# Performance work log

Measured on AMD Instinct MI355X. Metric: run time of the kernel, lower is better.

The kernel has to match this reference:

```python
import jax, jax.numpy as jnp
import numpy as np

B, LQ, D = 4, 10000, 256
HEADS, LVLS, PTS = 8, 1, 4
HW = 100
LIN = HW * HW


def setup_inputs() -> dict:
    key = jax.random.key(0)
    ks = jax.random.split(key, 14)
    s = 0.02
    ctr = jax.random.uniform(ks[2], (B, LQ, LVLS, 2), jnp.float32)
    wh = 0.05 + 0.2 * jax.random.uniform(ks[3], (B, LQ, LVLS, 2), jnp.float32)
    return {
        "query": jax.random.normal(ks[0], (B, LQ, D), jnp.float32),
        "reference_points": jnp.concatenate([ctr, wh], axis=-1),
        "input_flatten": jax.random.normal(ks[1], (B, LIN, D), jnp.float32),
        "input_spatial_shapes": jnp.array([[HW, HW]], jnp.int32),
        "input_level_start_index": jnp.zeros((LVLS,), jnp.int32),
        "input_padding_mask": jnp.zeros((B, LIN), jnp.bool_),
        "Wv": s * jax.random.normal(ks[4], (D, D), jnp.float32),
        "bv": jnp.zeros((D,), jnp.float32),
        "Woff": s * jax.random.normal(ks[5], (D, HEADS * LVLS * PTS * 2), jnp.float32),
        "boff": s * jax.random.normal(ks[6], (HEADS * LVLS * PTS * 2,), jnp.float32),
        "Wa": s * jax.random.normal(ks[7], (D, HEADS * LVLS * PTS), jnp.float32),
        "ba": jnp.zeros((HEADS * LVLS * PTS,), jnp.float32),
        "Wout": s * jax.random.normal(ks[8], (D, D), jnp.float32),
        "bout": jnp.zeros((D,), jnp.float32),
    }


def _ms_deform_attn(query, reference_points, input_flatten, input_padding_mask,
                    Wv, bv, Woff, boff, Wa, ba, Wout, bout):
    Bn, Lq, Dm = query.shape
    Lin = input_flatten.shape[1]
    Hh, L, P = HEADS, LVLS, PTS
    Cd = Dm // Hh
    # value projection + padding mask
    value = input_flatten @ Wv + bv
    value = jnp.where(input_padding_mask[..., None], 0.0, value)
    # sampling offsets & attention weights
    off = (query @ Woff + boff).reshape(Bn, Lq, Hh, L, P, 2)
    attn = jax.nn.softmax((query @ Wa + ba).reshape(Bn, Lq, Hh, L * P), axis=-1)
    loc = (reference_points[:, :, None, :, None, :2]
           + off / P * reference_points[:, :, None, :, None, 2:] * 0.5)
    # value -> (B*Hh, Cd, Lin); square single-level map H=W=sqrt(Lin)
    v = value.reshape(Bn, Lin, Hh, Cd).transpose(0, 2, 3, 1).reshape(Bn * Hh, Cd, Lin)
    Hs = int(round(Lin ** 0.5)); Ws = Hs
    # level 0 grid: (B*Hh, Lq, P, 2), normalized to [-1, 1]
    g = (2.0 * loc - 1.0)[:, :, :, 0].transpose(0, 2, 1, 3, 4).reshape(Bn * Hh, Lq, P, 2)
    x = (g[..., 0] + 1.0) * Ws / 2.0 - 0.5
    y = (g[..., 1] + 1.0) * Hs / 2.0 - 0.5
    x0 = jnp.floor(x).astype(jnp.int32); y0 = jnp.floor(y).astype(jnp.int32)
    x1 = x0 + 1; y1 = y0 + 1
    wx = x - x0.astype(x.dtype); wy = y - y0.astype(y.dtype)

    def valid(xi, yi):
        return ((xi >= 0) & (xi < Ws) & (yi >= 0) & (yi < Hs)).astype(value.dtype)

    def gather(xi, yi):
        idx = (jnp.clip(yi, 0, Hs - 1) * Ws + jnp.clip(xi, 0, Ws - 1)).reshape(Bn * Hh, 1, Lq * P)
        out = jnp.take_along_axis(v, jnp.broadcast_to(idx, (Bn * Hh, Cd, Lq * P)), axis=2)
        return out.reshape(Bn * Hh, Cd, Lq, P)

    sv = (gather(x0, y0) * ((1 - wx) * (1 - wy) * valid(x0, y0))[:, None]
          + gather(x0, y1) * ((1 - wx) * wy * valid(x0, y1))[:, None]
          + gather(x1, y0) * (wx * (1 - wy) * valid(x1, y0))[:, None]
          + gather(x1, y1) * (wx * wy * valid(x1, y1))[:, None])  # (B*Hh, Cd, Lq, P)
    aw = attn.transpose(0, 2, 1, 3).reshape(Bn * Hh, 1, Lq, L * P)
    out = (sv * aw).sum(-1).reshape(Bn, Hh * Cd, Lq).transpose(0, 2, 1)  # (B, Lq, D)
    return out @ Wout + bout


def reference(query, reference_points, input_flatten, input_spatial_shapes,
              input_level_start_index, input_padding_mask,
              Wv, bv, Woff, boff, Wa, ba, Wout, bout):
    # input_spatial_shapes / level_start_index are redundant here: the core is
    # single-level with H=W=sqrt(Len_in) (faithful to the source code).
    return _ms_deform_attn(query, reference_points, input_flatten, input_padding_mask,
                           Wv, bv, Woff, boff, Wa, ba, Wout, bout)
```

## Files before the change

kernel.cpp:

```cpp
#include <hip/hip_runtime.h>

#define BATCH 4
#define LQ    10000
#define DM    256
#define NH    8
#define NP    4
#define HWD   100
#define LIN   10000

typedef unsigned short ushort_t;
typedef __attribute__((ext_vector_type(8))) short bf16x8;
typedef __attribute__((ext_vector_type(8))) unsigned short u16x8;
typedef __attribute__((ext_vector_type(4))) float f32x4;

__device__ __forceinline__ unsigned short f2bf(float f) {
    unsigned int u = __float_as_uint(f);
    u += 0x7FFFu + ((u >> 16) & 1u);
    return (unsigned short)(u >> 16);
}

__device__ __forceinline__ void gload16(const ushort_t* g, ushort_t* l) {
    __builtin_amdgcn_global_load_lds(
        (const __attribute__((address_space(1))) void*)g,
        (__attribute__((address_space(3))) void*)l, 16, 0, 0);
}

__global__ __launch_bounds__(256) void prep_kernel(
    const float* __restrict__ Wv, const float* __restrict__ Wout,
    const float* __restrict__ Woff, const float* __restrict__ Wa,
    const float* __restrict__ boff, const float* __restrict__ ba,
    ushort_t* __restrict__ WtV, ushort_t* __restrict__ WtO,
    ushort_t* __restrict__ Wcomb, float* __restrict__ bcomb)
{
    const int n = blockIdx.x, k = threadIdx.x;
    const int t = k >> 6, lc = (k >> 3) & 7, j = k & 7;
    const int ct = lc ^ ((n >> 1) & 7);
    const size_t addr = (size_t)n * 256 + t * 64 + ct * 8 + j;
    if (blockIdx.y == 0) {
        WtV[addr] = f2bf(Wv[(size_t)k * 256 + n]);
    } else if (blockIdx.y == 1) {
        WtO[addr] = f2bf(Wout[(size_t)k * 256 + n]);
    } else if (n < 96) {
        float w = (n < 64) ? Woff[(size_t)k * 64 + n] : Wa[(size_t)k * 32 + (n - 64)];
        Wcomb[addr] = f2bf(w);
        if (k == 0) bcomb[n] = (n < 64) ? boff[n] : ba[n - 64];
    }
}

__global__ __launch_bounds__(256) void gemm_in_kernel(
    const float* __restrict__ flat, const float* __restrict__ query,
    const ushort_t* __restrict__ WtV, const ushort_t* __restrict__ Wcomb,
    const float* __restrict__ bv, const float* __restrict__ bcomb,
    ushort_t* __restrict__ value, float* __restrict__ oaproj)
{
    __shared__ ushort_t As[64 * 64];
    __shared__ ushort_t Bs[256 * 64];

    const int tid  = threadIdx.x;
    const int lane = tid & 63;
    const int wv   = tid >> 6;

    const int ar  = tid >> 2;
    const int akb = tid & 3;
    const int as_ = (ar >> 1) & 7;
    const int fr = lane & 15, kb = lane >> 4;
    const int ln8 = lane >> 3, lc8 = lane & 7;

    if (blockIdx.x < 625) {
        const int row0 = blockIdx.x * 64;
        const f32x4 zero = {0.f, 0.f, 0.f, 0.f};
        f32x4 acc[4][4];
        #pragma unroll
        for (int m = 0; m < 4; ++m)
            #pragma unroll
            for (int n = 0; n < 4; ++n) acc[m][n] = zero;

        for (int k0 = 0; k0 < 256; k0 += 64) {
            const int t = k0 >> 6;
            #pragma unroll
            for (int it = 0; it < 8; ++it) {
                int r0 = (it * 4 + wv) * 8;
                gload16(&WtV[(size_t)(r0 + ln8) * 256 + t * 64 + lc8 * 8],
                        &Bs[r0 * 64]);
            }
            {
                const float* p = &flat[(size_t)(row0 + ar) * 256 + k0 + akb * 8];
                float4 f0 = *reinterpret_cast<const float4*>(p);
                float4 f1 = *reinterpret_cast<const float4*>(p + 4);
                u16x8 pk;
                pk[0] = f2bf(f0.x); pk[1] = f2bf(f0.y);
                pk[2] = f2bf(f0.z); pk[3] = f2bf(f0.w);
                pk[4] = f2bf(f1.x); pk[5] = f2bf(f1.y);
                pk[6] = f2bf(f1.z); pk[7] = f2bf(f1.w);
                *reinterpret_cast<u16x8*>(&As[ar * 64 + ((akb ^ as_) * 8)]) = pk;
                f0 = *reinterpret_cast<const float4*>(p + 32);
                f1 = *reinterpret_cast<const float4*>(p + 36);
                pk[0] = f2bf(f0.x); pk[1] = f2bf(f0.y);
                pk[2] = f2bf(f0.z); pk[3] = f2bf(f0.w);
                pk[4] = f2bf(f1.x); pk[5] = f2bf(f1.y);
                pk[6] = f2bf(f1.z); pk[7] = f2bf(f1.w);
                *reinterpret_cast<u16x8*>(&As[ar * 64 + (((akb + 4) ^ as_) * 8)]) = pk;
            }
            __syncthreads();

            #pragma unroll
            for (int ks = 0; ks < 2; ++ks) {
                const int lc = ks * 4 + kb;
                bf16x8 af[4], bf[4];
                #pragma unroll
                for (int m = 0; m < 4; ++m) {
                    int r = m * 16 + fr;
                    af[m] = *reinterpret_cast<const bf16x8*>(
                        &As[r * 64 + ((lc ^ ((r >> 1) & 7)) * 8)]);
                }
                #pragma unroll
                for (int n = 0; n < 4; ++n) {
                    int c = wv * 64 + n * 16 + fr;
                    bf[n] = *reinterpret_cast<const bf16x8*>(
                        &Bs[c * 64 + ((lc ^ ((c >> 1) & 7)) * 8)]);
                }
                #pragma unroll
                for (int m = 0; m < 4; ++m)
                    #pragma unroll
                    for (int n = 0; n < 4; ++n)
                        acc[m][n] = __builtin_amdgcn_mfma_f32_16x16x32_bf16(
                            af[m], bf[n], acc[m][n], 0, 0, 0);
            }
            __syncthreads();
        }

        #pragma unroll
        for (int n = 0; n < 4; ++n) {
            int c = wv * 64 + n * 16 + fr;
            float bb = bv[c];
            int hh = c >> 5, ch = c & 31;
            #pragma unroll
            for (int m = 0; m < 4; ++m) {
                #pragma unroll
                for (int j = 0; j < 4; ++j) {
                    int r = row0 + m * 16 + kb * 4 + j;
                    int rb = (int)((unsigned)r / 10000u);
                    int pix = r - rb * 10000;
                    size_t addr = (((size_t)(rb * 8 + hh)) * LIN + pix) * 32 + ch;
                    value[addr] = f2bf(acc[m][n][j] + bb);
                }
            }
        }
    } else {
        const int row0 = (blockIdx.x - 625) * 64;
        const f32x4 zero = {0.f, 0.f, 0.f, 0.f};
        f32x4 acc[6];
        #pragma unroll
        for (int n = 0; n < 6; ++n) acc[n] = zero;

        for (int k0 = 0; k0 < 256; k0 += 64) {
            const int t = k0 >> 6;
            #pragma unroll
            for (int it = 0; it < 3; ++it) {
                int r0 = (it * 4 + wv) * 8;
                gload16(&Wcomb[(size_t)(r0 + ln8) * 256 + t * 64 + lc8 * 8],
                        &Bs[r0 * 64]);
            }
            {
                const float* p = &query[(size_t)(row0 + ar) * 256 + k0 + akb * 8];
                float4 f0 = *reinterpret_cast<const float4*>(p);
                float4 f1 = *reinterpret_cast<const float4*>(p + 4);
                u16x8 pk;
                pk[0] = f2bf(f0.x); pk[1] = f2bf(f0.y);
                pk[2] = f2bf(f0.z); pk[3] = f2bf(f0.w);
                pk[4] = f2bf(f1.x); pk[5] = f2bf(f1.y);
                pk[6] = f2bf(f1.z); pk[7] = f2bf(f1.w);
                *reinterpret_cast<u16x8*>(&As[ar * 64 + ((akb ^ as_) * 8)]) = pk;
                f0 = *reinterpret_cast<const float4*>(p + 32);
                f1 = *reinterpret_cast<const float4*>(p + 36);
                pk[0] = f2bf(f0.x); pk[1] = f2bf(f0.y);
                pk[2] = f2bf(f0.z); pk[3] = f2bf(f0.w);
                pk[4] = f2bf(f1.x); pk[5] = f2bf(f1.y);
                pk[6] = f2bf(f1.z); pk[7] = f2bf(f1.w);
                *reinterpret_cast<u16x8*>(&As[ar * 64 + (((akb + 4) ^ as_) * 8)]) = pk;
            }
            __syncthreads();

            #pragma unroll
            for (int ks = 0; ks < 2; ++ks) {
                const int lc = ks * 4 + kb;
                bf16x8 af;
                {
                    int r = wv * 16 + fr;
                    af = *reinterpret_cast<const bf16x8*>(
                        &As[r * 64 + ((lc ^ ((r >> 1) & 7)) * 8)]);
                }
                #pragma unroll
                for (int n = 0; n < 6; ++n) {
                    int c = n * 16 + fr;
                    bf16x8 bf = *reinterpret_cast<const bf16x8*>(
                        &Bs[c * 64 + ((lc ^ ((c >> 1) & 7)) * 8)]);
                    acc[n] = __builtin_amdgcn_mfma_f32_16x16x32_bf16(
                        af, bf, acc[n], 0, 0, 0);
                }
            }
            __syncthreads();
        }

        #pragma unroll
        for (int n = 0; n < 6; ++n) {
            int c = n * 16 + fr;
            float bb = bcomb[c];
            #pragma unroll
            for (int j = 0; j < 4; ++j) {
                int r = row0 + wv * 16 + kb * 4 + j;
                oaproj[(size_t)r * 96 + c] = acc[n][j] + bb;
            }
        }
    }
}

__global__ __launch_bounds__(256, 4) void deform_kernel(
    const float* __restrict__ oaproj, const float* __restrict__ refpts,
    const ushort_t* __restrict__ value, ushort_t* __restrict__ out)
{
    __shared__ int4   soff[NP * 64];
    __shared__ float4 swt [NP * 64];

    const int blk = blockIdx.x;
    const int xcd = blk & 7;
    const int sub = (blk >> 3) & 3;
    const int chunk = blk >> 5;
    const int map = xcd * 4 + sub;
    const int b = map >> 3, h = map & 7;
    const int q0 = chunk * 64;

    const int tid = threadIdx.x;

    if (tid < 64) {
        const int qg = q0 + tid;
        if (qg >= LQ) {
            int4 zi = {0, 0, 0, 0};
            float4 zf = {0.f, 0.f, 0.f, 0.f};
            #pragma unroll
            for (int p = 0; p < NP; ++p) { soff[p * 64 + tid] = zi; swt[p * 64 + tid] = zf; }
        } else {
            const size_t row = (size_t)b * LQ + qg;
            const float* oa = oaproj + row * 96;
            float4 l4 = *reinterpret_cast<const float4*>(oa + 64 + h * 4);
            float mx = fmaxf(fmaxf(l4.x, l4.y), fmaxf(l4.z, l4.w));
            float e0 = __expf(l4.x - mx), e1 = __expf(l4.y - mx);
            float e2 = __expf(l4.z - mx), e3 = __expf(l4.w - mx);
            float inv = 1.f / (e0 + e1 + e2 + e3);
            float ew[4] = {e0 * inv, e1 * inv, e2 * inv, e3 * inv};
            float4 o0 = *reinterpret_cast<const float4*>(oa + h * 8);
            float4 o1 = *reinterpret_cast<const float4*>(oa + h * 8 + 4);
            float oxv[4] = {o0.x, o0.z, o1.x, o1.z};
            float oyv[4] = {o0.y, o0.w, o1.y, o1.w};
            const float* rp = refpts + row * 4;
            float cx = rp[0], cy = rp[1], rw = rp[2], rh = rp[3];
            #pragma unroll
            for (int p = 0; p < NP; ++p) {
                float x = (cx + oxv[p] * rw * 0.125f) * (float)HWD - 0.5f;
                float y = (cy + oyv[p] * rh * 0.125f) * (float)HWD - 0.5f;
                float x0f = floorf(x), y0f = floorf(y);
                float wx = x - x0f, wy = y - y0f;
                int x0 = (int)x0f, y0 = (int)y0f;
                int x1 = x0 + 1, y1 = y0 + 1;
                float vx0 = (x0 >= 0 && x0 < HWD) ? 1.f : 0.f;
                float vx1 = (x1 >= 0 && x1 < HWD) ? 1.f : 0.f;
                float vy0 = (y0 >= 0 && y0 < HWD) ? 1.f : 0.f;
                float vy1 = (y1 >= 0 && y1 < HWD) ? 1.f : 0.f;
                int cx0 = min(max(x0, 0), HWD - 1), cx1 = min(max(x1, 0), HWD - 1);
                int cy0 = min(max(y0, 0), HWD - 1), cy1 = min(max(y1, 0), HWD - 1);
                float aw = ew[p];
                int4 of = {cy0 * HWD + cx0, cy0 * HWD + cx1,
                           cy1 * HWD + cx0, cy1 * HWD + cx1};
                float4 wt = {aw * (1.f - wx) * (1.f - wy) * vx0 * vy0,
                             aw * wx * (1.f - wy) * vx1 * vy0,
                             aw * (1.f - wx) * wy * vx0 * vy1,
                             aw * wx * wy * vx1 * vy1};
                soff[p * 64 + tid] = of;
                swt [p * 64 + tid] = wt;
            }
        }
    }
    __syncthreads();

    const int q = tid >> 2, c8 = tid & 3;
    const int qg = q0 + q;
    const ushort_t* vb = value + (size_t)map * (LIN * 32) + c8 * 8;

    int4 of[4]; float4 w4[4];
    #pragma unroll
    for (int p = 0; p < NP; ++p) {
        of[p] = soff[p * 64 + q];
        w4[p] = swt [p * 64 + q];
    }
    uint4 vv[4][4];
    #pragma unroll
    for (int p = 0; p < NP; ++p) {
        vv[p][0] = *reinterpret_cast<const uint4*>(vb + ((size_t)of[p].x << 5));
        vv[p][1] = *reinterpret_cast<const uint4*>(vb + ((size_t)of[p].y << 5));
        vv[p][2] = *reinterpret_cast<const uint4*>(vb + ((size_t)of[p].z << 5));
        vv[p][3] = *reinterpret_cast<const uint4*>(vb + ((size_t)of[p].w << 5));
    }
    float a0 = 0.f, a1 = 0.f, a2 = 0.f, a3 = 0.f;
    float a4 = 0.f, a5 = 0.f, a6 = 0.f, a7 = 0.f;
    #define ACC(V, W) { const float w_ = (W); const uint4 v_ = (V); \
        a0 += w_ * __uint_as_float(v_.x << 16); \
        a1 += w_ * __uint_as_float(v_.x & 0xffff0000u); \
        a2 += w_ * __uint_as_float(v_.y << 16); \
        a3 += w_ * __uint_as_float(v_.y & 0xffff0000u); \
        a4 += w_ * __uint_as_float(v_.z << 16); \
        a5 += w_ * __uint_as_float(v_.z & 0xffff0000u); \
        a6 += w_ * __uint_as_float(v_.w << 16); \
        a7 += w_ * __uint_as_float(v_.w & 0xffff0000u); }
    #pragma unroll
    for (int p = 0; p < NP; ++p) {
        ACC(vv[p][0], w4[p].x);
        ACC(vv[p][1], w4[p].y);
        ACC(vv[p][2], w4[p].z);
        ACC(vv[p][3], w4[p].w);
    }
    #undef ACC

    if (qg < LQ) {
        const size_t orow = (size_t)b * LQ + qg;
        u16x8 pk;
        pk[0] = f2bf(a0); pk[1] = f2bf(a1);
        pk[2] = f2bf(a2); pk[3] = f2bf(a3);
        pk[4] = f2bf(a4); pk[5] = f2bf(a5);
        pk[6] = f2bf(a6); pk[7] = f2bf(a7);
        const int cc = h * 4 + c8;
        const int t = cc >> 3;
        const int ct = (cc & 7) ^ ((int)(orow >> 1) & 7);
        *reinterpret_cast<u16x8*>(&out[orow * 256 + t * 64 + ct * 8]) = pk;
    }
}

__global__ __launch_bounds__(256) void gemm_out_kernel(
    const ushort_t* __restrict__ A, const ushort_t* __restrict__ Wt,
    const float* __restrict__ bias, float* __restrict__ Cout)
{
    __shared__ ushort_t As[64 * 64];
    __shared__ ushort_t Bs[256 * 64];

    const int tid  = threadIdx.x;
    const int lane = tid & 63;
    const int wv   = tid >> 6;
    const int row0 = blockIdx.x * 64;

    const f32x4 zero = {0.f, 0.f, 0.f, 0.f};
    f32x4 acc[4][4];
    #pragma unroll
    for (int m = 0; m < 4; ++m)
        #pragma unroll
        for (int n = 0; n < 4; ++n) acc[m][n] = zero;

    const int fr = lane & 15, kb = lane >> 4;
    const int ln8 = lane >> 3, lc8 = lane & 7;

    for (int k0 = 0; k0 < 256; k0 += 64) {
        const int t = k0 >> 6;
        #pragma unroll
        for (int it = 0; it < 2; ++it) {
            int r0 = (it * 4 + wv) * 8;
            gload16(&A[(size_t)(row0 + r0 + ln8) * 256 + t * 64 + lc8 * 8],
                    &As[r0 * 64]);
        }
        #pragma unroll
        for (int it = 0; it < 8; ++it) {
            int r0 = (it * 4 + wv) * 8;
            gload16(&Wt[(size_t)(r0 + ln8) * 256 + t * 64 + lc8 * 8],
                    &Bs[r0 * 64]);
        }
        __syncthreads();

        #pragma unroll
        for (int ks = 0; ks < 2; ++ks) {
            const int lc = ks * 4 + kb;
            bf16x8 af[4], bf[4];
            #pragma unroll
            for (int m = 0; m < 4; ++m) {
                int r = m * 16 + fr;
                af[m] = *reinterpret_cast<const bf16x8*>(
                    &As[r * 64 + ((lc ^ ((r >> 1) & 7)) * 8)]);
            }
            #pragma unroll
            for (int n = 0; n < 4; ++n) {
                int c = wv * 64 + n * 16 + fr;
                bf[n] = *reinterpret_cast<const bf16x8*>(
                    &Bs[c * 64 + ((lc ^ ((c >> 1) & 7)) * 8)]);
            }
            #pragma unroll
            for (int m = 0; m < 4; ++m)
                #pragma unroll
                for (int n = 0; n < 4; ++n)
                    acc[m][n] = __builtin_amdgcn_mfma_f32_16x16x32_bf16(
                        af[m], bf[n], acc[m][n], 0, 0, 0);
        }
        __syncthreads();
    }

    #pragma unroll
    for (int m = 0; m < 4; ++m) {
        #pragma unroll
        for (int n = 0; n < 4; ++n) {
            int c = wv * 64 + n * 16 + fr;
            float bb = bias[c];
            #pragma unroll
            for (int j = 0; j < 4; ++j) {
                int r = row0 + m * 16 + kb * 4 + j;
                Cout[(size_t)r * 256 + c] = acc[m][n][j] + bb;
            }
        }
    }
}

extern "C" void kernel_launch(void* const* d_in, const int* in_sizes, int n_in,
                              void* d_out, int out_size, void* d_ws, size_t ws_size,
                              hipStream_t stream)
{
    const float* query  = (const float*)d_in[0];
    const float* refpts = (const float*)d_in[1];
    const float* flat   = (const float*)d_in[2];
    const float* Wv   = (const float*)d_in[6];
    const float* bv   = (const float*)d_in[7];
    const float* Woff = (const float*)d_in[8];
    const float* boff = (const float*)d_in[9];
    const float* Wa   = (const float*)d_in[10];
    const float* ba   = (const float*)d_in[11];
    const float* Wout = (const float*)d_in[12];
    const float* bout = (const float*)d_in[13];
    float* out = (float*)d_out;

    const size_t MROWS = (size_t)BATCH * LIN;
    ushort_t* value  = (ushort_t*)d_ws;
    ushort_t* ws2    = value + MROWS * DM;
    ushort_t* WtV    = ws2 + MROWS * DM;
    ushort_t* WtO    = WtV + 256 * 256;
    ushort_t* Wcomb  = WtO + 256 * 256;
    float*    bcomb  = (float*)(Wcomb + 96 * 256);
    float*    oaproj = bcomb + 128;

    dim3 blk(256);

    prep_kernel<<<dim3(256, 3), blk, 0, stream>>>(
        Wv, Wout, Woff, Wa, boff, ba, WtV, WtO, Wcomb, bcomb);

    gemm_in_kernel<<<dim3(1250), blk, 0, stream>>>(
        flat, query, WtV, Wcomb, bv, bcomb, value, oaproj);

    deform_kernel<<<dim3(157 * 32), blk, 0, stream>>>(
        oaproj, refpts, value, ws2);

    gemm_out_kernel<<<dim3(MROWS / 64), blk, 0, stream>>>(
        ws2, WtO, bout, out);
}
```

Baseline: 72.71 us.

## Double-buffer GEMM K-tiles with 32-wide LDS stages and prefetch

Converts the input-projection and output-projection GEMMs from single-buffered 64-wide K tiles with two barriers per step to double-buffered 32-wide K tiles. The next tile's global loads are issued before the MFMAs on the current one, so memory latency overlaps compute and one barrier per step is dropped. The weight pre-swizzle and the sampler's output layout change to the 32-wide swizzle to match. This adds more loop iterations and barriers in total, and keeps LDS usage the same.

```diff
diff --git a/kernel.cpp b/kernel.cpp
--- a/kernel.cpp
+++ b/kernel.cpp
@@ -33,9 +33,9 @@
     ushort_t* __restrict__ Wcomb, float* __restrict__ bcomb)
 {
     const int n = blockIdx.x, k = threadIdx.x;
-    const int t = k >> 6, lc = (k >> 3) & 7, j = k & 7;
-    const int ct = lc ^ ((n >> 1) & 7);
-    const size_t addr = (size_t)n * 256 + t * 64 + ct * 8 + j;
+    const int t32 = k >> 5, lc = (k >> 3) & 3, j = k & 7;
+    const int ct = lc ^ ((n >> 1) & 3);
+    const size_t addr = (size_t)n * 256 + t32 * 32 + ct * 8 + j;
     if (blockIdx.y == 0) {
         WtV[addr] = f2bf(Wv[(size_t)k * 256 + n]);
     } else if (blockIdx.y == 1) {
@@ -53,8 +53,8 @@
     const float* __restrict__ bv, const float* __restrict__ bcomb,
     ushort_t* __restrict__ value, float* __restrict__ oaproj)
 {
-    __shared__ ushort_t As[64 * 64];
-    __shared__ ushort_t Bs[256 * 64];
+    __shared__ ushort_t As[2][64 * 32];
+    __shared__ ushort_t Bs[2][256 * 32];
 
     const int tid  = threadIdx.x;
     const int lane = tid & 63;
@@ -62,12 +62,13 @@
 
     const int ar  = tid >> 2;
     const int akb = tid & 3;
-    const int as_ = (ar >> 1) & 7;
+    const int asw = (akb ^ ((ar >> 1) & 3)) * 8;
     const int fr = lane & 15, kb = lane >> 4;
-    const int ln8 = lane >> 3, lc8 = lane & 7;
+    const int ln4 = lane >> 2, lc4 = lane & 3;
 
     if (blockIdx.x < 625) {
         const int row0 = blockIdx.x * 64;
+        const float* ap = &flat[(size_t)(row0 + ar) * 256 + akb * 8];
         const f32x4 zero = {0.f, 0.f, 0.f, 0.f};
         f32x4 acc[4][4];
         #pragma unroll
@@ -75,65 +76,74 @@
             #pragma unroll
             for (int n = 0; n < 4; ++n) acc[m][n] = zero;
 
-        for (int k0 = 0; k0 < 256; k0 += 64) {
-            const int t = k0 >> 6;
-            #pragma unroll
-            for (int it = 0; it < 8; ++it) {
-                int r0 = (it * 4 + wv) * 8;
-                gload16(&WtV[(size_t)(r0 + ln8) * 256 + t * 64 + lc8 * 8],
-                        &Bs[r0 * 64]);
-            }
-            {
-                const float* p = &flat[(size_t)(row0 + ar) * 256 + k0 + akb * 8];
-                float4 f0 = *reinterpret_cast<const float4*>(p);
-                float4 f1 = *reinterpret_cast<const float4*>(p + 4);
+        {
+            float4 f0 = *reinterpret_cast<const float4*>(ap);
+            float4 f1 = *reinterpret_cast<const float4*>(ap + 4);
+            u16x8 pk;
+            pk[0] = f2bf(f0.x); pk[1] = f2bf(f0.y);
+            pk[2] = f2bf(f0.z); pk[3] = f2bf(f0.w);
+            pk[4] = f2bf(f1.x); pk[5] = f2bf(f1.y);
+            pk[6] = f2bf(f1.z); pk[7] = f2bf(f1.w);
+            *reinterpret_cast<u16x8*>(&As[0][ar * 32 + asw]) = pk;
+            #pragma unroll
+            for (int it = 0; it < 4; ++it) {
+                int r0 = (it * 4 + wv) * 16;
+                gload16(&WtV[(size_t)(r0 + ln4) * 256 + lc4 * 8], &Bs[0][r0 * 32]);
+            }
+        }
+        __syncthreads();
+
+        int c = 0;
+        for (int t = 0; t < 8; ++t) {
+            const int kn = (t + 1) * 32;
+            const bool pf = (t < 7);
+            float4 f0, f1;
+            if (pf) {
+                f0 = *reinterpret_cast<const float4*>(ap + kn);
+                f1 = *reinterpret_cast<const float4*>(ap + kn + 4);
+                #pragma unroll
+                for (int it = 0; it < 4; ++it) {
+                    int r0 = (it * 4 + wv) * 16;
+                    gload16(&WtV[(size_t)(r0 + ln4) * 256 + kn + lc4 * 8],
+                            &Bs[c ^ 1][r0 * 32]);
+                }
+            }
+            bf16x8 af[4], bf[4];
+            #pragma unroll
+            for (int m = 0; m < 4; ++m) {
+                int r = m * 16 + fr;
+                af[m] = *reinterpret_cast<const bf16x8*>(
+                    &As[c][r * 32 + ((kb ^ ((r >> 1) & 3)) * 8)]);
+            }
+            #pragma unroll
+            for (int n = 0; n < 4; ++n) {
+                int cc = wv * 64 + n * 16 + fr;
+                bf[n] = *reinterpret_cast<const bf16x8*>(
+                    &Bs[c][cc * 32 + ((kb ^ ((cc >> 1) & 3)) * 8)]);
+            }
+            #pragma unroll
+            for (int m = 0; m < 4; ++m)
+                #pragma unroll
+                for (int n = 0; n < 4; ++n)
+                    acc[m][n] = __builtin_amdgcn_mfma_f32_16x16x32_bf16(
+                        af[m], bf[n], acc[m][n], 0, 0, 0);
+            if (pf) {
                 u16x8 pk;
                 pk[0] = f2bf(f0.x); pk[1] = f2bf(f0.y);
                 pk[2] = f2bf(f0.z); pk[3] = f2bf(f0.w);
                 pk[4] = f2bf(f1.x); pk[5] = f2bf(f1.y);
                 pk[6] = f2bf(f1.z); pk[7] = f2bf(f1.w);
-                *reinterpret_cast<u16x8*>(&As[ar * 64 + ((akb ^ as_) * 8)]) = pk;
-                f0 = *reinterpret_cast<const float4*>(p + 32);
-                f1 = *reinterpret_cast<const float4*>(p + 36);
-                pk[0] = f2bf(f0.x); pk[1] = f2bf(f0.y);
-                pk[2] = f2bf(f0.z); pk[3] = f2bf(f0.w);
-                pk[4] = f2bf(f1.x); pk[5] = f2bf(f1.y);
-                pk[6] = f2bf(f1.z); pk[7] = f2bf(f1.w);
-                *reinterpret_cast<u16x8*>(&As[ar * 64 + (((akb + 4) ^ as_) * 8)]) = pk;
+                *reinterpret_cast<u16x8*>(&As[c ^ 1][ar * 32 + asw]) = pk;
             }
             __syncthreads();
-
-            #pragma unroll
-            for (int ks = 0; ks < 2; ++ks) {
-                const int lc = ks * 4 + kb;
-                bf16x8 af[4], bf[4];
-                #pragma unroll
-                for (int m = 0; m < 4; ++m) {
-                    int r = m * 16 + fr;
-                    af[m] = *reinterpret_cast<const bf16x8*>(
-                        &As[r * 64 + ((lc ^ ((r >> 1) & 7)) * 8)]);
-                }
-                #pragma unroll
-                for (int n = 0; n < 4; ++n) {
-                    int c = wv * 64 + n * 16 + fr;
-                    bf[n] = *reinterpret_cast<const bf16x8*>(
-                        &Bs[c * 64 + ((lc ^ ((c >> 1) & 7)) * 8)]);
-                }
-                #pragma unroll
-                for (int m = 0; m < 4; ++m)
-                    #pragma unroll
-                    for (int n = 0; n < 4; ++n)
-                        acc[m][n] = __builtin_amdgcn_mfma_f32_16x16x32_bf16(
-                            af[m], bf[n], acc[m][n], 0, 0, 0);
-            }
-            __syncthreads();
+            c ^= 1;
         }
 
         #pragma unroll
         for (int n = 0; n < 4; ++n) {
-            int c = wv * 64 + n * 16 + fr;
-            float bb = bv[c];
-            int hh = c >> 5, ch = c & 31;
+            int cc = wv * 64 + n * 16 + fr;
+            float bb = bv[cc];
+            int hh = cc >> 5, ch = cc & 31;
             #pragma unroll
             for (int m = 0; m < 4; ++m) {
                 #pragma unroll
@@ -148,68 +158,80 @@
         }
     } else {
         const int row0 = (blockIdx.x - 625) * 64;
+        const float* ap = &query[(size_t)(row0 + ar) * 256 + akb * 8];
         const f32x4 zero = {0.f, 0.f, 0.f, 0.f};
         f32x4 acc[6];
         #pragma unroll
         for (int n = 0; n < 6; ++n) acc[n] = zero;
 
-        for (int k0 = 0; k0 < 256; k0 += 64) {
-            const int t = k0 >> 6;
-            #pragma unroll
-            for (int it = 0; it < 3; ++it) {
-                int r0 = (it * 4 + wv) * 8;
-                gload16(&Wcomb[(size_t)(r0 + ln8) * 256 + t * 64 + lc8 * 8],
-                        &Bs[r0 * 64]);
-            }
+        {
+            float4 f0 = *reinterpret_cast<const float4*>(ap);
+            float4 f1 = *reinterpret_cast<const float4*>(ap + 4);
+            u16x8 pk;
+            pk[0] = f2bf(f0.x); pk[1] = f2bf(f0.y);
+            pk[2] = f2bf(f0.z); pk[3] = f2bf(f0.w);
+            pk[4] = f2bf(f1.x); pk[5] = f2bf(f1.y);
+            pk[6] = f2bf(f1.z); pk[7] = f2bf(f1.w);
+            *reinterpret_cast<u16x8*>(&As[0][ar * 32 + asw]) = pk;
+            #pragma unroll
+            for (int it = 0; it < 2; ++it) {
+                int r0 = (it * 4 + wv) * 16;
+                if (r0 < 96)
+                    gload16(&Wcomb[(size_t)(r0 + ln4) * 256 + lc4 * 8], &Bs[0][r0 * 32]);
+            }
+        }
+        __syncthreads();
+
+        int c = 0;
+        for (int t = 0; t < 8; ++t) {
+            const int kn = (t + 1) * 32;
+            const bool pf = (t < 7);
+            float4 f0, f1;
+            if (pf) {
+                f0 = *reinterpret_cast<const float4*>(ap + kn);
+                f1 = *reinterpret_cast<const float4*>(ap + kn + 4);
+                #pragma unroll
+                for (int it = 0; it < 2; ++it) {
+                    int r0 = (it * 4 + wv) * 16;
+                    if (r0 < 96)
+                        gload16(&Wcomb[(size_t)(r0 + ln4) * 256 + kn + lc4 * 8],
+                                &Bs[c ^ 1][r0 * 32]);
+                }
+            }
+            bf16x8 af;
             {
-                const float* p = &query[(size_t)(row0 + ar) * 256 + k0 + akb * 8];
-                float4 f0 = *reinterpret_cast<const float4*>(p);
-                float4 f1 = *reinterpret_cast<const float4*>(p + 4);
+                int r = wv * 16 + fr;
+                af = *reinterpret_cast<const bf16x8*>(
+                    &As[c][r * 32 + ((kb ^ ((r >> 1) & 3)) * 8)]);
+            }
+            #pragma unroll
+            for (int n = 0; n < 6; ++n) {
+                int cc = n * 16 + fr;
+                bf16x8 bf = *reinterpret_cast<const bf16x8*>(
+                    &Bs[c][cc * 32 + ((kb ^ ((cc >> 1) & 3)) * 8)]);
+                acc[n] = __builtin_amdgcn_mfma_f32_16x16x32_bf16(
+                    af, bf, acc[n], 0, 0, 0);
+            }
+            if (pf) {
                 u16x8 pk;
                 pk[0] = f2bf(f0.x); pk[1] = f2bf(f0.y);
                 pk[2] = f2bf(f0.z); pk[3] = f2bf(f0.w);
                 pk[4] = f2bf(f1.x); pk[5] = f2bf(f1.y);
                 pk[6] = f2bf(f1.z); pk[7] = f2bf(f1.w);
-                *reinterpret_cast<u16x8*>(&As[ar * 64 + ((akb ^ as_) * 8)]) = pk;
-                f0 = *reinterpret_cast<const float4*>(p + 32);
-                f1 = *reinterpret_cast<const float4*>(p + 36);
-                pk[0] = f2bf(f0.x); pk[1] = f2bf(f0.y);
-                pk[2] = f2bf(f0.z); pk[3] = f2bf(f0.w);
-                pk[4] = f2bf(f1.x); pk[5] = f2bf(f1.y);
-                pk[6] = f2bf(f1.z); pk[7] = f2bf(f1.w);
-                *reinterpret_cast<u16x8*>(&As[ar * 64 + (((akb + 4) ^ as_) * 8)]) = pk;
+                *reinterpret_cast<u16x8*>(&As[c ^ 1][ar * 32 + asw]) = pk;
             }
             __syncthreads();
-
-            #pragma unroll
-            for (int ks = 0; ks < 2; ++ks) {
-                const int lc = ks * 4 + kb;
-                bf16x8 af;
-                {
-                    int r = wv * 16 + fr;
-                    af = *reinterpret_cast<const bf16x8*>(
-                        &As[r * 64 + ((lc ^ ((r >> 1) & 7)) * 8)]);
-                }
-                #pragma unroll
-                for (int n = 0; n < 6; ++n) {
-                    int c = n * 16 + fr;
-                    bf16x8 bf = *reinterpret_cast<const bf16x8*>(
-                        &Bs[c * 64 + ((lc ^ ((c >> 1) & 7)) * 8)]);
-                    acc[n] = __builtin_amdgcn_mfma_f32_16x16x32_bf16(
-                        af, bf, acc[n], 0, 0, 0);
-                }
-            }
-            __syncthreads();
+            c ^= 1;
         }
 
         #pragma unroll
         for (int n = 0; n < 6; ++n) {
-            int c = n * 16 + fr;
-            float bb = bcomb[c];
+            int cc = n * 16 + fr;
+            float bb = bcomb[cc];
             #pragma unroll
             for (int j = 0; j < 4; ++j) {
                 int r = row0 + wv * 16 + kb * 4 + j;
-                oaproj[(size_t)r * 96 + c] = acc[n][j] + bb;
+                oaproj[(size_t)r * 96 + cc] = acc[n][j] + bb;
             }
         }
     }
@@ -328,9 +350,9 @@
         pk[4] = f2bf(a4); pk[5] = f2bf(a5);
         pk[6] = f2bf(a6); pk[7] = f2bf(a7);
         const int cc = h * 4 + c8;
-        const int t = cc >> 3;
-        const int ct = (cc & 7) ^ ((int)(orow >> 1) & 7);
-        *reinterpret_cast<u16x8*>(&out[orow * 256 + t * 64 + ct * 8]) = pk;
+        const int t32 = cc >> 2;
+        const int ct = (cc & 3) ^ ((int)(orow >> 1) & 3);
+        *reinterpret_cast<u16x8*>(&out[orow * 256 + t32 * 32 + ct * 8]) = pk;
     }
 }
 
@@ -338,8 +360,8 @@
     const ushort_t* __restrict__ A, const ushort_t* __restrict__ Wt,
     const float* __restrict__ bias, float* __restrict__ Cout)
 {
-    __shared__ ushort_t As[64 * 64];
-    __shared__ ushort_t Bs[256 * 64];
+    __shared__ ushort_t As[2][64 * 32];
+    __shared__ ushort_t Bs[2][256 * 32];
 
     const int tid  = threadIdx.x;
     const int lane = tid & 63;
@@ -354,60 +376,65 @@
         for (int n = 0; n < 4; ++n) acc[m][n] = zero;
 
     const int fr = lane & 15, kb = lane >> 4;
-    const int ln8 = lane >> 3, lc8 = lane & 7;
-
-    for (int k0 = 0; k0 < 256; k0 += 64) {
-        const int t = k0 >> 6;
-        #pragma unroll
-        for (int it = 0; it < 2; ++it) {
-            int r0 = (it * 4 + wv) * 8;
-            gload16(&A[(size_t)(row0 + r0 + ln8) * 256 + t * 64 + lc8 * 8],
-                    &As[r0 * 64]);
-        }
-        #pragma unroll
-        for (int it = 0; it < 8; ++it) {
-            int r0 = (it * 4 + wv) * 8;
-            gload16(&Wt[(size_t)(r0 + ln8) * 256 + t * 64 + lc8 * 8],
-                    &Bs[r0 * 64]);
-        }
+    const int ln4 = lane >> 2, lc4 = lane & 3;
+
+    {
+        gload16(&A[(size_t)(row0 + wv * 16 + ln4) * 256 + lc4 * 8],
+                &As[0][wv * 512]);
+        #pragma unroll
+        for (int it = 0; it < 4; ++it) {
+            int r0 = (it * 4 + wv) * 16;
+            gload16(&Wt[(size_t)(r0 + ln4) * 256 + lc4 * 8], &Bs[0][r0 * 32]);
+        }
+    }
+    __syncthreads();
+
+    int c = 0;
+    for (int t = 0; t < 8; ++t) {
+        const int kn = (t + 1) * 32;
+        if (t < 7) {
+            gload16(&A[(size_t)(row0 + wv * 16 + ln4) * 256 + kn + lc4 * 8],
+                    &As[c ^ 1][wv * 512]);
+            #pragma unroll
+            for (int it = 0; it < 4; ++it) {
+                int r0 = (it * 4 + wv) * 16;
+                gload16(&Wt[(size_t)(r0 + ln4) * 256 + kn + lc4 * 8],
+                        &Bs[c ^ 1][r0 * 32]);
+            }
+        }
+        bf16x8 af[4], bf[4];
+        #pragma unroll
+        for (int m = 0; m < 4; ++m) {
+            int r = m * 16 + fr;
+            af[m] = *reinterpret_cast<const bf16x8*>(
+                &As[c][r * 32 + ((kb ^ ((r >> 1) & 3)) * 8)]);
+        }
+        #pragma unroll
+        for (int n = 0; n < 4; ++n) {
+            int cc = wv * 64 + n * 16 + fr;
+            bf[n] = *reinterpret_cast<const bf16x8*>(
+                &Bs[c][cc * 32 + ((kb ^ ((cc >> 1) & 3)) * 8)]);
+        }
+        #pragma unroll
+        for (int m = 0; m < 4; ++m)
+            #pragma unroll
+            for (int n = 0; n < 4; ++n)
+                acc[m][n] = __builtin_amdgcn_mfma_f32_16x16x32_bf16(
+                    af[m], bf[n], acc[m][n], 0, 0, 0);
         __syncthreads();
-
-        #pragma unroll
-        for (int ks = 0; ks < 2; ++ks) {
-            const int lc = ks * 4 + kb;
-            bf16x8 af[4], bf[4];
-            #pragma unroll
-            for (int m = 0; m < 4; ++m) {
-                int r = m * 16 + fr;
-                af[m] = *reinterpret_cast<const bf16x8*>(
-                    &As[r * 64 + ((lc ^ ((r >> 1) & 7)) * 8)]);
-            }
-            #pragma unroll
-            for (int n = 0; n < 4; ++n) {
-                int c = wv * 64 + n * 16 + fr;
-                bf[n] = *reinterpret_cast<const bf16x8*>(
-                    &Bs[c * 64 + ((lc ^ ((c >> 1) & 7)) * 8)]);
-            }
-            #pragma unroll
-            for (int m = 0; m < 4; ++m)
-                #pragma unroll
-                for (int n = 0; n < 4; ++n)
-                    acc[m][n] = __builtin_amdgcn_mfma_f32_16x16x32_bf16(
-                        af[m], bf[n], acc[m][n], 0, 0, 0);
-        }
-        __syncthreads();
+        c ^= 1;
     }
 
     #pragma unroll
     for (int m = 0; m < 4; ++m) {
         #pragma unroll
         for (int n = 0; n < 4; ++n) {
-            int c = wv * 64 + n * 16 + fr;
-            float bb = bias[c];
+            int cc = wv * 64 + n * 16 + fr;
+            float bb = bias[cc];
             #pragma unroll
             for (int j = 0; j < 4; ++j) {
                 int r = row0 + m * 16 + kb * 4 + j;
-                Cout[(size_t)r * 256 + c] = acc[m][n][j] + bb;
+                Cout[(size_t)r * 256 + cc] = acc[m][n][j] + bb;
             }
         }
     }
```

New measurement: 70.91 us. 1.03x faster.
